# Performance work log

Hardware: AMD Instinct MI355X
Metric: run time of the kernel (lower is better)

The kernel has to match this reference:

```python
import jax, jax.numpy as jnp
import numpy as np
import math

CYCLES = [5, 6, 7, 8]


def gamaka_pe(T, D):
    pos = np.arange(T, dtype=np.float32)[:, None]
    div = np.exp(np.arange(0, D, 2, dtype=np.float32) * (-math.log(10000.0) / D))
    pe = np.zeros((T, D), np.float32)
    pe[:, 0::2] = np.sin(pos * div)
    pe[:, 1::2] = np.cos(pos * div[: D // 2])
    tala = np.zeros((T, D), np.float32)
    slots = D // 4
    half = slots // 2
    harm = np.arange(1, half + 1, dtype=np.float32)
    for t_idx, c in enumerate(CYCLES):
        phase = (pos % c) / c * 2.0 * math.pi
        s = t_idx * slots
        tala[:, s:s + half] = np.sin(phase * harm)
        tala[:, s + half:s + slots] = np.cos(phase * harm)
    return jnp.asarray(0.5 * pe + 0.5 * tala)


def layer_norm(x, g, b, eps=1e-5):
    m = x.mean(-1, keepdims=True)
    v = ((x - m) ** 2).mean(-1, keepdims=True)
    return (x - m) / jnp.sqrt(v + eps) * g + b


def gru_all_threads(x, wih, whh, bih, bhh):
    # x:(B,T,D), wih/whh:(4,3D,D), bih/bhh:(4,3D) -> (4,B,T,D)
    xp = jnp.einsum('kij,btj->kbti', wih, x) + bih[:, None, None, :]  # (4,B,T,3D)
    K, B, T, _ = xp.shape
    D = x.shape[-1]

    def step(h, xt):  # h:(4,B,D), xt:(4,B,3D)
        gh = jnp.einsum('kij,kbj->kbi', whh, h) + bhh[:, None, :]
        xr, xz, xn = jnp.split(xt, 3, axis=-1)
        hr, hz, hn = jnp.split(gh, 3, axis=-1)
        r = jax.nn.sigmoid(xr + hr)
        z = jax.nn.sigmoid(xz + hz)
        n = jnp.tanh(xn + r * hn)
        h = (1.0 - z) * n + z * h
        return h, h

    h0 = jnp.zeros((K, B, D), x.dtype)
    _, hs = jax.lax.scan(step, h0, jnp.moveaxis(xp, 2, 0))  # (T,4,B,D)
    return jnp.moveaxis(hs, 0, 2)  # (4,B,T,D)


def setup_inputs() -> dict:
    key = jax.random.key(0)
    ks = jax.random.split(key, 16)
    B, T, D = 4, 2048, 512
    s = 0.02
    return {
        'x': jax.random.normal(ks[0], (B, T, D), jnp.float32),
        'gru_wih': s * jax.random.normal(ks[1], (4, 3 * D, D), jnp.float32),
        'gru_whh': s * jax.random.normal(ks[2], (4, 3 * D, D), jnp.float32),
        'gru_bih': s * jax.random.normal(ks[3], (4, 3 * D), jnp.float32),
        'gru_bhh': s * jax.random.normal(ks[4], (4, 3 * D), jnp.float32),
        'wq': s * jax.random.normal(ks[5], (4, D, D), jnp.float32),
        'wk': s * jax.random.normal(ks[6], (4, D, D), jnp.float32),
        'wv': s * jax.random.normal(ks[7], (4, D, D), jnp.float32),
        'w_beat': s * jax.random.normal(ks[8], (4, D, 2 * D), jnp.float32),
        'norm_g': jnp.ones((4, D), jnp.float32),
        'norm_b': jnp.zeros((4, D), jnp.float32),
        'w_mix': s * jax.random.normal(ks[9], (D, 4 * D), jnp.float32),
        'bn_g': jnp.ones((D,), jnp.float32),
        'bn_b': jnp.zeros((D,), jnp.float32),
    }


def reference(x, gru_wih, gru_whh, gru_bih, gru_bhh, wq, wk, wv, w_beat,
              norm_g, norm_b, w_mix, bn_g, bn_b):
    B, T, D = x.shape
    x = x + gamaka_pe(T, D)[None]

    gru_out = gru_all_threads(x, gru_wih, gru_whh, gru_bih, gru_bhh)  # (4,B,T,D)

    q = jnp.einsum('kij,btj->kbti', wq, x)
    k = jnp.einsum('kij,btj->kbti', wk, x)
    v = jnp.einsum('kij,btj->kbti', wv, x)

    idx = jnp.arange(T)
    diff = idx[:, None] - idx[None, :]  # (T,T)
    cyc = jnp.asarray(CYCLES)[:, None, None]
    valid = (diff[None] >= 0) & (diff[None] < cyc)  # (4,T,T)
    mask = jnp.where(valid, 0.0, -jnp.inf).astype(x.dtype)

    scores = jnp.einsum('kbtd,kbsd->kbts', q, k) / jnp.sqrt(jnp.asarray(D, x.dtype))
    attn = jax.nn.softmax(scores + mask[:, None], axis=-1)
    attn_out = jnp.einsum('kbts,kbsd->kbtd', attn, v)

    comb = jnp.concatenate([gru_out, attn_out], axis=-1)  # (4,B,T,2D)
    beat = jnp.einsum('kij,kbtj->kbti', w_beat, comb)
    thr = layer_norm(beat + x[None], norm_g[:, None, None, :], norm_b[:, None, None, :])

    merged = jnp.moveaxis(thr, 0, 2).reshape(B, T, 4 * D)  # concat thread order 0..3
    out = jnp.einsum('ij,btj->bti', w_mix, merged)
    return layer_norm(out + x, bn_g, bn_b)
```

## Files before the change

### kernel.cpp

```cpp
#include <hip/hip_runtime.h>
#include <hip/hip_bf16.h>
#include <math.h>


using frag8   = __attribute__((ext_vector_type(8))) short;
using floatx4 = __attribute__((ext_vector_type(4))) float;

#define B_ 4
#define T_ 2048
#define D_ 512
#define BT_ (B_ * T_)

static __device__ __forceinline__ float bf2f(unsigned short u) {
    return __uint_as_float(((unsigned)u) << 16);
}
static __device__ __forceinline__ unsigned short f2bfbits(float f) {
    unsigned u = __float_as_uint(f);
    u = (u + 0x7FFF + ((u >> 16) & 1)) >> 16;
    return (unsigned short)u;
}

static __device__ __forceinline__ float pe_tala(int t, int d) {
    int i2 = d >> 1;
    const float c0 = (float)(-9.210340371976184 / 512.0);
    float dv = expf((float)(2 * i2) * c0);
    float a  = (float)t * dv;
    float pe = (d & 1) ? cosf(a) : sinf(a);
    int kk = d >> 7;
    int s  = d & 127;
    int c  = kk + 5;
    float phase = ((float)(t % c) / (float)c) * 6.2831854820251465f;
    float harm  = (float)((s & 63) + 1);
    float ta = (s < 64) ? sinf(phase * harm) : cosf(phase * harm);
    return 0.5f * pe + 0.5f * ta;
}

__global__ void k_fill(float* __restrict__ out, int n) {
    int i = blockIdx.x * 256 + threadIdx.x;
    if (i < n) out[i] = 1234.5f;
}

__global__ void k_prep(const float* __restrict__ x, __hip_bfloat16* __restrict__ xinbf)
{
    int idx = blockIdx.x * 256 + threadIdx.x;
    if (idx >= B_ * T_ * D_) return;
    int d = idx & 511;
    int t = (idx >> 9) & 2047;
    xinbf[idx] = __float2bfloat16(x[idx] + pe_tala(t, d));
}

__global__ void k_f2bf(const float* __restrict__ src, __hip_bfloat16* __restrict__ dst, int n)
{
    int i = blockIdx.x * 256 + threadIdx.x;
    if (i < n) dst[i] = __float2bfloat16(src[i]);
}

__global__ __launch_bounds__(256) void k_gemm(
    const __hip_bfloat16* __restrict__ A, const __hip_bfloat16* __restrict__ B,
    float* __restrict__ Cf, __hip_bfloat16* __restrict__ Cb,
    const float* __restrict__ bias, const __hip_bfloat16* __restrict__ resid,
    int M, int N, int K,
    long sA_, long sB_, long sC_, long sBias_)
{
    const int bz = blockIdx.z;
    A += (size_t)bz * sA_;
    B += (size_t)bz * sB_;
    const float* biasp = bias ? bias + (size_t)bz * sBias_ : (const float*)0;

    const int m0 = blockIdx.x * 128, n0 = blockIdx.y * 128;
    const int tid  = threadIdx.x;
    const int lane = tid & 63, wv = tid >> 6;
    const int wm = (wv >> 1) * 64, wn = (wv & 1) * 64;
    const int fr = lane & 15, quad = lane >> 4;

    __shared__ __align__(16) __hip_bfloat16 sAt[128 * 32];
    __shared__ __align__(16) __hip_bfloat16 sBt[128 * 32];

    floatx4 acc[4][4];
#pragma unroll
    for (int mi = 0; mi < 4; mi++)
#pragma unroll
        for (int ni = 0; ni < 4; ni++) acc[mi][ni] = (floatx4){0.f, 0.f, 0.f, 0.f};

    const int srow = tid >> 2;
    const int scol = (tid & 3) * 8;

    for (int k0 = 0; k0 < K; k0 += 32) {
        frag8 av0 = *(const frag8*)(A + (size_t)(m0 +      srow) * K + (k0 + scol));
        frag8 av1 = *(const frag8*)(A + (size_t)(m0 + 64 + srow) * K + (k0 + scol));
        frag8 bv0 = *(const frag8*)(B + (size_t)(n0 +      srow) * K + (k0 + scol));
        frag8 bv1 = *(const frag8*)(B + (size_t)(n0 + 64 + srow) * K + (k0 + scol));
        __syncthreads();
        *(frag8*)&sAt[(     srow) * 32 + scol] = av0;
        *(frag8*)&sAt[(64 + srow) * 32 + scol] = av1;
        *(frag8*)&sBt[(     srow) * 32 + scol] = bv0;
        *(frag8*)&sBt[(64 + srow) * 32 + scol] = bv1;
        __syncthreads();

        frag8 af[4], bfr[4];
#pragma unroll
        for (int mi = 0; mi < 4; mi++)
            af[mi] = *(const frag8*)&sAt[(wm + mi * 16 + fr) * 32 + quad * 8];
#pragma unroll
        for (int ni = 0; ni < 4; ni++)
            bfr[ni] = *(const frag8*)&sBt[(wn + ni * 16 + fr) * 32 + quad * 8];
#pragma unroll
        for (int mi = 0; mi < 4; mi++)
#pragma unroll
            for (int ni = 0; ni < 4; ni++)
                acc[mi][ni] = __builtin_amdgcn_mfma_f32_16x16x32_bf16(af[mi], bfr[ni], acc[mi][ni], 0, 0, 0);
    }

    const size_t coff = (size_t)bz * sC_;
#pragma unroll
    for (int mi = 0; mi < 4; mi++) {
#pragma unroll
        for (int ni = 0; ni < 4; ni++) {
            const int col = n0 + wn + ni * 16 + fr;
            const float bval = biasp ? biasp[col] : 0.f;
#pragma unroll
            for (int r2 = 0; r2 < 4; r2++) {
                const int row = m0 + wm + mi * 16 + quad * 4 + r2;
                const size_t ci = (size_t)row * N + col;
                float v = acc[mi][ni][r2] + bval;
                if (resid) v += bf2f(((const unsigned short*)resid)[ci]);
                if (Cf) Cf[coff + ci] = v;
                else    Cb[coff + ci] = __float2bfloat16(v);
            }
        }
    }
}

__global__ __launch_bounds__(256) void k_attn(
    const __hip_bfloat16* __restrict__ Q, const __hip_bfloat16* __restrict__ Kx,
    const __hip_bfloat16* __restrict__ Vx, __hip_bfloat16* __restrict__ comb)
{
    const int pair = blockIdx.y;
    const int kk = pair >> 2;
    const int c = kk + 5;
    const int t0 = blockIdx.x * 16;
    const int tid = threadIdx.x, lane = tid & 63, wv = tid >> 6;

    __shared__ __align__(16) unsigned short kls[23 * 512];
    __shared__ __align__(16) unsigned short vls[23 * 512];

    const size_t qb = (size_t)pair * T_ * D_;
    for (int e = tid; e < 23 * 64; e += 256) {
        int r = e >> 6, ce = (e & 63) << 3;
        int s = t0 - 7 + r;
        frag8 kv = (frag8){0,0,0,0,0,0,0,0};
        frag8 vv = kv;
        if (s >= 0) {
            kv = *(const frag8*)((const unsigned short*)Kx + qb + (size_t)s * 512 + ce);
            vv = *(const frag8*)((const unsigned short*)Vx + qb + (size_t)s * 512 + ce);
        }
        *(frag8*)&kls[r * 512 + ce] = kv;
        *(frag8*)&vls[r * 512 + ce] = vv;
    }
    __syncthreads();

    const float scale = 0.044194173824159216f;
    for (int tt = wv; tt < 16; tt += 4) {
        const int t = t0 + tt;
        float qv[8];
        const unsigned short* qrow = (const unsigned short*)Q + qb + (size_t)t * 512 + lane * 8;
#pragma unroll
        for (int i = 0; i < 8; i++) qv[i] = bf2f(qrow[i]);

        float sc[8];
#pragma unroll
        for (int si = 0; si < 8; ++si) {
            const int s = t - 7 + si;
            const int r = tt + si;
            const unsigned short* krow = &kls[r * 512 + lane * 8];
            float p = 0.f;
#pragma unroll
            for (int i = 0; i < 8; i++) p += qv[i] * bf2f(krow[i]);
#pragma unroll
            for (int off = 1; off < 64; off <<= 1) p += __shfl_xor(p, off);
            const bool valid = (s >= 0) && (s >= t - c + 1);
            sc[si] = valid ? p * scale : -1e30f;
        }
        float mx = -1e30f;
#pragma unroll
        for (int si = 0; si < 8; ++si) mx = fmaxf(mx, sc[si]);
        float sum = 0.f;
#pragma unroll
        for (int si = 0; si < 8; ++si) { sc[si] = expf(sc[si] - mx); sum += sc[si]; }
        const float inv = 1.f / sum;

        float o[8] = {0,0,0,0,0,0,0,0};
#pragma unroll
        for (int si = 0; si < 8; ++si) {
            const int r = tt + si;
            const float w = sc[si] * inv;
            const unsigned short* vrow = &vls[r * 512 + lane * 8];
#pragma unroll
            for (int i = 0; i < 8; i++) o[i] += w * bf2f(vrow[i]);
        }
        frag8 ov;
#pragma unroll
        for (int i = 0; i < 8; i++) ov[i] = (short)f2bfbits(o[i]);
        *(frag8*)((unsigned short*)comb + ((size_t)pair * T_ + t) * 1024 + 512 + lane * 8) = ov;
    }
}

__global__ __launch_bounds__(512, 2) void k_gru(
    const float* __restrict__ whh, const float* __restrict__ bhh,
    const __hip_bfloat16* __restrict__ xp,
    unsigned long long* __restrict__ hbuf,
    __hip_bfloat16* __restrict__ comb)
{
    const int pair = blockIdx.x & 15;
    const int wg   = blockIdx.x >> 4;
    const int kk   = pair >> 2;
    const int tid  = threadIdx.x;
    const int g = tid >> 4, j = tid & 15;
    const int d = wg * 32 + g;

    const float* wbase = whh + (size_t)kk * 1536 * 512;
    float4 wr4[8], wz4[8], wn4[8];
#pragma unroll
    for (int q = 0; q < 8; q++) {
        const int e = j * 32 + ((q ^ j) & 7) * 4;
        wr4[q] = *(const float4*)(wbase + (size_t)d * 512 + e);
        wz4[q] = *(const float4*)(wbase + (size_t)(512 + d) * 512 + e);
        wn4[q] = *(const float4*)(wbase + (size_t)(1024 + d) * 512 + e);
    }
    const float bhr = bhh[kk * 1536 + d];
    const float bhz = bhh[kk * 1536 + 512 + d];
    const float bhn = bhh[kk * 1536 + 1024 + d];

    const unsigned short* xbase = (const unsigned short*)xp + (size_t)pair * T_ * 1536;
    __shared__ __align__(16) float h_lds[2][512];

    int bail = 0;
    for (int t = 0; t < T_; ++t) {
        const int par = t & 1;
        const unsigned short* xrow = xbase + (size_t)t * 1536;
        float xr = 0.f, xz = 0.f, xn = 0.f;
        if (j == 0) {
            xr = bf2f(xrow[d]);
            xz = bf2f(xrow[512 + d]);
            xn = bf2f(xrow[1024 + d]);
        }

        if (t == 0) {
            h_lds[0][tid] = 0.f;
        } else {
            unsigned long long* hrow = hbuf + ((size_t)pair * 4 + ((t - 1) & 3)) * 512;
            const unsigned tag = (unsigned)t;
            unsigned long long a0;
            for (;;) {
                a0 = __hip_atomic_load(&hrow[tid], __ATOMIC_RELAXED, __HIP_MEMORY_SCOPE_AGENT);
                if ((unsigned)(a0 >> 32) == tag) break;
                if (++bail > 2000000) break;
            }
            h_lds[par][tid] = __uint_as_float((unsigned)a0);
        }
        __syncthreads();

        float ar = 0.f, az = 0.f, an = 0.f;
#pragma unroll
        for (int q = 0; q < 8; q++) {
            const int e = j * 32 + ((q ^ j) & 7) * 4;
            const float4 h4 = *(const float4*)&h_lds[par][e];
            ar += wr4[q].x * h4.x + wr4[q].y * h4.y + wr4[q].z * h4.z + wr4[q].w * h4.w;
            az += wz4[q].x * h4.x + wz4[q].y * h4.y + wz4[q].z * h4.z + wz4[q].w * h4.w;
            an += wn4[q].x * h4.x + wn4[q].y * h4.y + wn4[q].z * h4.z + wn4[q].w * h4.w;
        }
#pragma unroll
        for (int off = 1; off < 16; off <<= 1) {
            ar += __shfl_xor(ar, off);
            az += __shfl_xor(az, off);
            an += __shfl_xor(an, off);
        }
        if (j == 0) {
            const float r = 1.f / (1.f + expf(-(xr + ar + bhr)));
            const float z = 1.f / (1.f + expf(-(xz + az + bhz)));
            const float n = tanhf(xn + r * (an + bhn));
            const float hprev = h_lds[par][d];
            const float hnew = (1.f - z) * n + z * hprev;
            const unsigned long long u =
                ((unsigned long long)(unsigned)(t + 1) << 32) | (unsigned long long)__float_as_uint(hnew);
            __hip_atomic_store(&hbuf[((size_t)pair * 4 + (t & 3)) * 512 + d], u,
                               __ATOMIC_RELAXED, __HIP_MEMORY_SCOPE_AGENT);
            comb[((size_t)pair * T_ + t) * 1024 + d] = __float2bfloat16(hnew);
        }
    }
}

__global__ void k_ln_thr(const __hip_bfloat16* __restrict__ bp,
                         const float* __restrict__ gg, const float* __restrict__ bb2,
                         __hip_bfloat16* __restrict__ thrm)
{
    const int kk = blockIdx.y;
    const int lane = threadIdx.x & 63, wv = threadIdx.x >> 6;
    float g8[8], b8[8];
#pragma unroll
    for (int i = 0; i < 8; i++) {
        g8[i] = gg[kk * 512 + lane * 8 + i];
        b8[i] = bb2[kk * 512 + lane * 8 + i];
    }
    for (int rr = 0; rr < 8; ++rr) {
        const int bt = blockIdx.x * 32 + wv * 8 + rr;
        const unsigned short* row = (const unsigned short*)bp + ((size_t)kk * BT_ + bt) * 512 + lane * 8;
        float v[8];
#pragma unroll
        for (int i = 0; i < 8; i++) v[i] = bf2f(row[i]);
        float s = 0.f, s2 = 0.f;
#pragma unroll
        for (int i = 0; i < 8; i++) { s += v[i]; s2 += v[i] * v[i]; }
#pragma unroll
        for (int off = 1; off < 64; off <<= 1) { s += __shfl_xor(s, off); s2 += __shfl_xor(s2, off); }
        const float mean = s * (1.f / 512.f);
        const float var = s2 * (1.f / 512.f) - mean * mean;
        const float rs = 1.f / sqrtf(var + 1e-5f);
        frag8 ov;
#pragma unroll
        for (int i = 0; i < 8; i++) ov[i] = (short)f2bfbits((v[i] - mean) * rs * g8[i] + b8[i]);
        *(frag8*)((unsigned short*)thrm + (size_t)bt * 2048 + kk * 512 + lane * 8) = ov;
    }
}

__global__ void k_ln_fin(const float* __restrict__ mo, const float* __restrict__ x,
                         const float* __restrict__ gg, const float* __restrict__ bb2,
                         float* __restrict__ out)
{
    const int lane = threadIdx.x & 63, wv = threadIdx.x >> 6;
    float g8[8], b8[8];
#pragma unroll
    for (int i = 0; i < 8; i++) {
        g8[i] = gg[lane * 8 + i];
        b8[i] = bb2[lane * 8 + i];
    }
    for (int rr = 0; rr < 8; ++rr) {
        const int bt = blockIdx.x * 32 + wv * 8 + rr;
        const int t = bt & 2047;
        const float* r1 = mo + (size_t)bt * 512 + lane * 8;
        const float* r2 = x + (size_t)bt * 512 + lane * 8;
        float v[8];
#pragma unroll
        for (int i = 0; i < 8; i++) v[i] = r1[i] + r2[i] + pe_tala(t, lane * 8 + i);
        float s = 0.f, s2 = 0.f;
#pragma unroll
        for (int i = 0; i < 8; i++) { s += v[i]; s2 += v[i] * v[i]; }
#pragma unroll
        for (int off = 1; off < 64; off <<= 1) { s += __shfl_xor(s, off); s2 += __shfl_xor(s2, off); }
        const float mean = s * (1.f / 512.f);
        const float var = s2 * (1.f / 512.f) - mean * mean;
        const float rs = 1.f / sqrtf(var + 1e-5f);
#pragma unroll
        for (int i = 0; i < 8; i++)
            out[(size_t)bt * 512 + lane * 8 + i] = (v[i] - mean) * rs * g8[i] + b8[i];
    }
}

extern "C" void kernel_launch(void* const* d_in, const int* in_sizes, int n_in,
                              void* d_out, int out_size, void* d_ws, size_t ws_size,
                              hipStream_t stream)
{
    const float* x     = (const float*)d_in[0];
    const float* wih   = (const float*)d_in[1];
    const float* whh   = (const float*)d_in[2];
    const float* bih   = (const float*)d_in[3];
    const float* bhh   = (const float*)d_in[4];
    const float* wq    = (const float*)d_in[5];
    const float* wk    = (const float*)d_in[6];
    const float* wv    = (const float*)d_in[7];
    const float* wbeat = (const float*)d_in[8];
    const float* ng    = (const float*)d_in[9];
    const float* nb    = (const float*)d_in[10];
    const float* wmix  = (const float*)d_in[11];
    const float* bng   = (const float*)d_in[12];
    const float* bnb   = (const float*)d_in[13];

    char* ws = (char*)d_ws;
    size_t off = 0;
    auto alloc = [&](size_t b) { size_t o = off; off += (b + 255) & ~(size_t)255; return o; };

    const size_t XINBF  = alloc((size_t)BT_ * 512 * 2);
    const size_t WIHBF  = alloc((size_t)4 * 1536 * 512 * 2);
    const size_t WQBF   = alloc((size_t)4 * 512 * 512 * 2);
    const size_t WKBF   = alloc((size_t)4 * 512 * 512 * 2);
    const size_t WVBF   = alloc((size_t)4 * 512 * 512 * 2);
    const size_t WBEATBF= alloc((size_t)4 * 512 * 1024 * 2);
    const size_t WMIXBF = alloc((size_t)512 * 2048 * 2);
    const size_t HBUF   = alloc((size_t)16 * 4 * 512 * 8);
    const size_t COMB   = alloc((size_t)4 * BT_ * 1024 * 2);
    const size_t BIG    = alloc((size_t)4 * BT_ * 1536 * 2);
    const size_t NEED   = off;

    const size_t XPO   = BIG;
    const size_t QO    = BIG;
    const size_t KO    = BIG + 33554432;
    const size_t VO    = BIG + 67108864;
    const size_t BEATO = BIG;
    const size_t THRO  = BIG + 33554432;
    const size_t MIXO  = BIG + 67108864;

    if (ws_size < NEED) {
        k_fill<<<(out_size + 255) / 256, 256, 0, stream>>>((float*)d_out, out_size);
        return;
    }

    hipMemsetAsync(ws + HBUF, 0, (size_t)16 * 4 * 512 * 8, stream);

    k_prep<<<(B_ * T_ * D_ + 255) / 256, 256, 0, stream>>>(x, (__hip_bfloat16*)(ws + XINBF));

    auto cast = [&](const float* s, size_t o, int n) {
        k_f2bf<<<(n + 255) / 256, 256, 0, stream>>>(s, (__hip_bfloat16*)(ws + o), n);
    };
    cast(wih,   WIHBF,  4 * 1536 * 512);
    cast(wq,    WQBF,   4 * 512 * 512);
    cast(wk,    WKBF,   4 * 512 * 512);
    cast(wv,    WVBF,   4 * 512 * 512);
    cast(wbeat, WBEATBF,4 * 512 * 1024);
    cast(wmix,  WMIXBF, 512 * 2048);

    const __hip_bfloat16* xinbf = (const __hip_bfloat16*)(ws + XINBF);

    k_gemm<<<dim3(BT_ / 128, 1536 / 128, 4), 256, 0, stream>>>(
        xinbf, (const __hip_bfloat16*)(ws + WIHBF),
        nullptr, (__hip_bfloat16*)(ws + XPO),
        bih, nullptr, BT_, 1536, 512,
        0, (long)1536 * 512, (long)BT_ * 1536, 1536);

    k_gru<<<256, 512, 0, stream>>>(
        whh, bhh, (const __hip_bfloat16*)(ws + XPO),
        (unsigned long long*)(ws + HBUF), (__hip_bfloat16*)(ws + COMB));

    k_gemm<<<dim3(BT_ / 128, 4, 4), 256, 0, stream>>>(
        xinbf, (const __hip_bfloat16*)(ws + WQBF), nullptr, (__hip_bfloat16*)(ws + QO),
        nullptr, nullptr, BT_, 512, 512, 0, (long)512 * 512, (long)BT_ * 512, 0);
    k_gemm<<<dim3(BT_ / 128, 4, 4), 256, 0, stream>>>(
        xinbf, (const __hip_bfloat16*)(ws + WKBF), nullptr, (__hip_bfloat16*)(ws + KO),
        nullptr, nullptr, BT_, 512, 512, 0, (long)512 * 512, (long)BT_ * 512, 0);
    k_gemm<<<dim3(BT_ / 128, 4, 4), 256, 0, stream>>>(
        xinbf, (const __hip_bfloat16*)(ws + WVBF), nullptr, (__hip_bfloat16*)(ws + VO),
        nullptr, nullptr, BT_, 512, 512, 0, (long)512 * 512, (long)BT_ * 512, 0);

    k_attn<<<dim3(T_ / 16, 16), 256, 0, stream>>>(
        (const __hip_bfloat16*)(ws + QO), (const __hip_bfloat16*)(ws + KO),
        (const __hip_bfloat16*)(ws + VO), (__hip_bfloat16*)(ws + COMB));

    k_gemm<<<dim3(BT_ / 128, 4, 4), 256, 0, stream>>>(
        (const __hip_bfloat16*)(ws + COMB), (const __hip_bfloat16*)(ws + WBEATBF),
        nullptr, (__hip_bfloat16*)(ws + BEATO),
        nullptr, xinbf, BT_, 512, 1024,
        (long)BT_ * 1024, (long)512 * 1024, (long)BT_ * 512, 0);

    k_ln_thr<<<dim3(BT_ / 32, 4), 256, 0, stream>>>(
        (const __hip_bfloat16*)(ws + BEATO), ng, nb, (__hip_bfloat16*)(ws + THRO));

    k_gemm<<<dim3(BT_ / 128, 4, 1), 256, 0, stream>>>(
        (const __hip_bfloat16*)(ws + THRO), (const __hip_bfloat16*)(ws + WMIXBF),
        (float*)(ws + MIXO), nullptr,
        nullptr, nullptr, BT_, 512, 2048, 0, 0, 0, 0);

    k_ln_fin<<<BT_ / 32, 256, 0, stream>>>(
        (const float*)(ws + MIXO), x, bng, bnb, (float*)d_out);
}
```

Measured before the change: 3.750 ms.

## Remap GRU recurrence to one wave per four outputs with DPP reductions

Restructures the persistent GRU step kernel so each wave owns four hidden units and all 64 lanes split the 512-long dot product, reading h with two contiguous float4 loads instead of swizzled chunks. Cross-lane reduction uses DPP row operations in place of shuffle-based xor reductions, and the previous hidden value is kept in a register instead of being reread from LDS. Weight registers are pinned with empty asm to keep them resident. The goal is to shorten the per-timestep critical path of the serial recurrence, at the cost of twelve full-wave reductions per step and more register pressure.

```diff
diff --git a/kernel.cpp b/kernel.cpp
--- a/kernel.cpp
+++ b/kernel.cpp
@@ -11,6 +11,9 @@
 #define D_ 512
 #define BT_ (B_ * T_)
 
+#define PIN4(v) asm volatile("" : "+v"((v).x), "+v"((v).y), "+v"((v).z), "+v"((v).w))
+#define PIN1(v) asm volatile("" : "+v"(v))
+
 static __device__ __forceinline__ float bf2f(unsigned short u) {
     return __uint_as_float(((unsigned)u) << 16);
 }
@@ -18,6 +21,21 @@
     unsigned u = __float_as_uint(f);
     u = (u + 0x7FFF + ((u >> 16) & 1)) >> 16;
     return (unsigned short)u;
+}
+
+template <int CTRL, int RM>
+static __device__ __forceinline__ float dpp_add(float x) {
+    int m = __builtin_amdgcn_update_dpp(0, __float_as_int(x), CTRL, RM, 0xF, true);
+    return x + __int_as_float(m);
+}
+static __device__ __forceinline__ float wave_red_sum64(float x) {
+    x = dpp_add<0xB1, 0xF>(x);
+    x = dpp_add<0x4E, 0xF>(x);
+    x = dpp_add<0x124, 0xF>(x);
+    x = dpp_add<0x128, 0xF>(x);
+    x = dpp_add<0x142, 0xA>(x);
+    x = dpp_add<0x143, 0xC>(x);
+    return x;
 }
 
 static __device__ __forceinline__ float pe_tala(int t, int d) {
@@ -208,38 +226,53 @@
 __global__ __launch_bounds__(512, 2) void k_gru(
     const float* __restrict__ whh, const float* __restrict__ bhh,
     const __hip_bfloat16* __restrict__ xp,
-    unsigned long long* __restrict__ hbuf,
+    unsigned long long* __restrict__ ring,
     __hip_bfloat16* __restrict__ comb)
 {
     const int pair = blockIdx.x & 15;
     const int wg   = blockIdx.x >> 4;
-    const int kk   = pair >> 2;
+    const int k    = pair >> 2;
     const int tid  = threadIdx.x;
-    const int g = tid >> 4, j = tid & 15;
-    const int d = wg * 32 + g;
-
-    const float* wbase = whh + (size_t)kk * 1536 * 512;
-    float4 wr4[8], wz4[8], wn4[8];
-#pragma unroll
-    for (int q = 0; q < 8; q++) {
-        const int e = j * 32 + ((q ^ j) & 7) * 4;
-        wr4[q] = *(const float4*)(wbase + (size_t)d * 512 + e);
-        wz4[q] = *(const float4*)(wbase + (size_t)(512 + d) * 512 + e);
-        wn4[q] = *(const float4*)(wbase + (size_t)(1024 + d) * 512 + e);
-    }
-    const float bhr = bhh[kk * 1536 + d];
-    const float bhz = bhh[kk * 1536 + 512 + d];
-    const float bhn = bhh[kk * 1536 + 1024 + d];
+    const int w    = tid >> 6;
+    const int j    = tid & 63;
+    const int dbase = wg * 32 + w * 4;
+
+    const float* wb = whh + (size_t)k * 1536 * 512;
+    float4 wv4[4][3][2];
+#pragma unroll
+    for (int dd = 0; dd < 4; dd++)
+#pragma unroll
+        for (int G = 0; G < 3; G++) {
+            const float* row = wb + (size_t)(G * 512 + dbase + dd) * 512;
+            wv4[dd][G][0] = *(const float4*)(row + 4 * j);
+            wv4[dd][G][1] = *(const float4*)(row + 256 + 4 * j);
+            PIN4(wv4[dd][G][0]);
+            PIN4(wv4[dd][G][1]);
+        }
+
+    const int isprod = (j >= 48) & (j < 52);
+    const int d = dbase + (j & 3);
+    float bhr = 0.f, bhz = 0.f, bhn = 0.f;
+    if (isprod) {
+        bhr = bhh[k * 1536 + d];
+        bhz = bhh[k * 1536 + 512 + d];
+        bhn = bhh[k * 1536 + 1024 + d];
+    }
+    PIN1(bhr); PIN1(bhz); PIN1(bhn);
+    float hcar = 0.f;
 
     const unsigned short* xbase = (const unsigned short*)xp + (size_t)pair * T_ * 1536;
+    unsigned long long* ringp = ring + (size_t)pair * 4 * 512;
+
     __shared__ __align__(16) float h_lds[2][512];
 
     int bail = 0;
     for (int t = 0; t < T_; ++t) {
         const int par = t & 1;
-        const unsigned short* xrow = xbase + (size_t)t * 1536;
+
         float xr = 0.f, xz = 0.f, xn = 0.f;
-        if (j == 0) {
+        if (isprod) {
+            const unsigned short* xrow = xbase + (size_t)t * 1536;
             xr = bf2f(xrow[d]);
             xz = bf2f(xrow[512 + d]);
             xn = bf2f(xrow[1024 + d]);
@@ -248,11 +281,11 @@
         if (t == 0) {
             h_lds[0][tid] = 0.f;
         } else {
-            unsigned long long* hrow = hbuf + ((size_t)pair * 4 + ((t - 1) & 3)) * 512;
+            unsigned long long* wp = ringp + (size_t)((t - 1) & 3) * 512 + tid;
             const unsigned tag = (unsigned)t;
             unsigned long long a0;
             for (;;) {
-                a0 = __hip_atomic_load(&hrow[tid], __ATOMIC_RELAXED, __HIP_MEMORY_SCOPE_AGENT);
+                a0 = __hip_atomic_load(wp, __ATOMIC_RELAXED, __HIP_MEMORY_SCOPE_AGENT);
                 if ((unsigned)(a0 >> 32) == tag) break;
                 if (++bail > 2000000) break;
             }
@@ -260,30 +293,36 @@
         }
         __syncthreads();
 
-        float ar = 0.f, az = 0.f, an = 0.f;
-#pragma unroll
-        for (int q = 0; q < 8; q++) {
-            const int e = j * 32 + ((q ^ j) & 7) * 4;
-            const float4 h4 = *(const float4*)&h_lds[par][e];
-            ar += wr4[q].x * h4.x + wr4[q].y * h4.y + wr4[q].z * h4.z + wr4[q].w * h4.w;
-            az += wz4[q].x * h4.x + wz4[q].y * h4.y + wz4[q].z * h4.z + wz4[q].w * h4.w;
-            an += wn4[q].x * h4.x + wn4[q].y * h4.y + wn4[q].z * h4.z + wn4[q].w * h4.w;
-        }
-#pragma unroll
-        for (int off = 1; off < 16; off <<= 1) {
-            ar += __shfl_xor(ar, off);
-            az += __shfl_xor(az, off);
-            an += __shfl_xor(an, off);
-        }
-        if (j == 0) {
+        const float4 h0 = *(const float4*)&h_lds[par][4 * j];
+        const float4 h1 = *(const float4*)&h_lds[par][256 + 4 * j];
+
+        float pr[12];
+#pragma unroll
+        for (int dd = 0; dd < 4; dd++)
+#pragma unroll
+            for (int G = 0; G < 3; G++) {
+                const float4 a = wv4[dd][G][0], b4 = wv4[dd][G][1];
+                pr[dd * 3 + G] =
+                    a.x * h0.x + a.y * h0.y + a.z * h0.z + a.w * h0.w +
+                    b4.x * h1.x + b4.y * h1.y + b4.z * h1.z + b4.w * h1.w;
+            }
+#pragma unroll
+        for (int i = 0; i < 12; i++) pr[i] = wave_red_sum64(pr[i]);
+
+        if (isprod) {
+            const int dd = j & 3;
+            const float ar = (dd & 2) ? ((dd & 1) ? pr[9]  : pr[6]) : ((dd & 1) ? pr[3]  : pr[0]);
+            const float az = (dd & 2) ? ((dd & 1) ? pr[10] : pr[7]) : ((dd & 1) ? pr[4]  : pr[1]);
+            const float an = (dd & 2) ? ((dd & 1) ? pr[11] : pr[8]) : ((dd & 1) ? pr[5]  : pr[2]);
             const float r = 1.f / (1.f + expf(-(xr + ar + bhr)));
             const float z = 1.f / (1.f + expf(-(xz + az + bhz)));
             const float n = tanhf(xn + r * (an + bhn));
-            const float hprev = h_lds[par][d];
-            const float hnew = (1.f - z) * n + z * hprev;
+            const float hnew = (1.f - z) * n + z * hcar;
+            hcar = hnew;
             const unsigned long long u =
-                ((unsigned long long)(unsigned)(t + 1) << 32) | (unsigned long long)__float_as_uint(hnew);
-            __hip_atomic_store(&hbuf[((size_t)pair * 4 + (t & 3)) * 512 + d], u,
+                ((unsigned long long)(unsigned)(t + 1) << 32) |
+                (unsigned long long)__float_as_uint(hnew);
+            __hip_atomic_store(&ringp[(size_t)(t & 3) * 512 + d], u,
                                __ATOMIC_RELAXED, __HIP_MEMORY_SCOPE_AGENT);
             comb[((size_t)pair * T_ + t) * 1024 + d] = __float2bfloat16(hnew);
         }
```

Result: slower. 4.644 ms (+23.9%).
